# Kernel tuning notes

Measured on AMD Instinct MI355X. Metric: run time of the kernel, lower is better.

Reference implementation:

```python
import jax, jax.numpy as jnp
import numpy as np

N = 100000
E = 1600000
D = 128      # input_dim == hidden_dim
C = 40       # output_dim
L = 3        # num_layers
EPS = 1e-12  # F.normalize eps


def setup_inputs() -> dict:
    key = jax.random.key(0)
    ks = jax.random.split(key, 8)
    x = jax.random.normal(ks[0], (N, D), dtype=jnp.float32)
    edge_index = jax.random.randint(ks[1], (2, E), 0, N, dtype=jnp.int64)
    s = 1.0 / np.sqrt(D)
    # SAGEConv: lin_l (neighbor path, with bias), lin_r (root path, no bias)
    Wl = jax.random.uniform(ks[2], (L, D, D), jnp.float32, -s, s)
    bl = jax.random.uniform(ks[3], (L, D), jnp.float32, -s, s)
    Wr = jax.random.uniform(ks[4], (L, D, D), jnp.float32, -s, s)
    Wlin = jax.random.uniform(ks[5], (C, D), jnp.float32, -s, s)
    blin = jax.random.uniform(ks[6], (C,), jnp.float32, -s, s)
    return {"x": x, "edge_index": edge_index, "Wl": Wl, "bl": bl,
            "Wr": Wr, "Wlin": Wlin, "blin": blin}


def reference(x, edge_index, Wl, bl, Wr, Wlin, blin):
    src, dst = edge_index[0], edge_index[1]
    # in-degree counts for mean aggregation (computed once, reused per layer)
    cnt = jax.ops.segment_sum(jnp.ones((E,), jnp.float32), dst, num_segments=N)
    inv_cnt = (1.0 / jnp.maximum(cnt, 1.0))[:, None]  # [N,1]
    z = x
    for i in range(L):
        msg = z[src]  # gather [E, D]
        agg = jax.ops.segment_sum(msg, dst, num_segments=N) * inv_cnt  # mean [N, D]
        out = agg @ Wl[i].T + bl[i] + z @ Wr[i].T
        # SAGEConv normalize=True: L2 normalize per node
        nrm = jnp.linalg.norm(out, axis=-1, keepdims=True)
        out = out / jnp.maximum(nrm, EPS)
        z = jax.nn.relu(out)  # dropout p=0 -> identity
    return z @ Wlin.T + blin  # [N, C]
```

## Files before the change

### kernel.cpp

```cpp
#include <hip/hip_runtime.h>


typedef __bf16 bf16x8 __attribute__((ext_vector_type(8)));
typedef float  f32x4  __attribute__((ext_vector_type(4)));

#define MFMA16(a, b, c) __builtin_amdgcn_mfma_f32_16x16x32_bf16((a), (b), (c), 0, 0, 0)

__device__ __forceinline__ unsigned rne_bf16(float f) {
  unsigned u = __float_as_uint(f);
  unsigned r = u + 0x7FFFu + ((u >> 16) & 1u);
  return r >> 16;
}

__device__ __forceinline__ float bf_lo(unsigned u) { return __uint_as_float(u << 16); }
__device__ __forceinline__ float bf_hi(unsigned u) { return __uint_as_float(u & 0xFFFF0000u); }

__global__ __launch_bounds__(256) void prep_k(
    const float* __restrict__ x, const float* __restrict__ Wl,
    const float* __restrict__ Wr, const float* __restrict__ Wlin,
    uint2* __restrict__ planeA, unsigned short* __restrict__ wfrag,
    unsigned short* __restrict__ wlf, int* __restrict__ gcur,
    int cap, int n4) {
  const int b = blockIdx.x;
  const int tid = threadIdx.x;
  if (b == 0) {
    if (tid < 128) gcur[tid] = tid * cap;
    return;
  }
  if (b <= 96) {
    int id = (b - 1) * 256 + tid;
    int l = id & 63;
    int c = (id >> 6) & 7;
    int t = (id >> 9) & 7;
    int p = (id >> 12) & 1;
    int layer = id >> 13;
    int col = t * 16 + (l & 15);
    int kbase = c * 32 + (l >> 4) * 8;
    unsigned short* dst = wfrag + (size_t)layer * 65536 +
                          ((((size_t)p * 8 + t) * 8 + c) * 64 + l) * 8;
#pragma unroll
    for (int j = 0; j < 8; ++j) {
      int k = kbase + j;
      float w = (k < 128) ? Wl[layer * 16384 + col * 128 + k]
                          : Wr[layer * 16384 + col * 128 + (k - 128)];
      unsigned h = rne_bf16(w);
      unsigned o;
      if (p == 0) o = h;
      else o = rne_bf16(w - __uint_as_float(h << 16));
      dst[j] = (unsigned short)o;
    }
    return;
  }
  if (b == 97) {
    for (int id = tid; id < 3 * 4 * 64; id += 256) {
      int l = id & 63;
      int c = (id >> 6) & 3;
      int t = id >> 8;
      int col = t * 16 + (l & 15);
      int kbase = c * 32 + (l >> 4) * 8;
      unsigned short* dst = wlf + (size_t)id * 8;
#pragma unroll
      for (int j = 0; j < 8; ++j) {
        float w = (col < 40) ? Wlin[col * 128 + kbase + j] : 0.f;
        dst[j] = (unsigned short)rne_bf16(w);
      }
    }
    return;
  }
  int i = (b - 98) * 256 + tid;
  if (i >= n4) return;
  float4 f = ((const float4*)x)[i];
  uint2 o;
  o.x = rne_bf16(f.x) | (rne_bf16(f.y) << 16);
  o.y = rne_bf16(f.z) | (rne_bf16(f.w) << 16);
  planeA[i] = o;
}


__global__ __launch_bounds__(256) void bucketA_k(
    const int* __restrict__ src, const int* __restrict__ dst,
    int* __restrict__ gcur, unsigned* __restrict__ coarse, int E, int nc) {
  __shared__ int hist[128];
  __shared__ int sd[128];
  __shared__ int lpos[128];
  __shared__ int gbase[128];
  __shared__ unsigned stage[2048];
  __shared__ unsigned char sbuck[2048];

  const int tid = threadIdx.x;
  const int e0 = blockIdx.x * 2048;

  if (tid < 128) hist[tid] = 0;
  __syncthreads();

  int bv[8], pk[8];
#pragma unroll
  for (int j = 0; j < 8; ++j) {
    int e = e0 + j * 256 + tid;
    bv[j] = -1;
    if (e < E) {
      int s = src[e], d = dst[e];
      bv[j] = d >> 10;
      pk[j] = s | ((d & 1023) << 17);
      atomicAdd(&hist[bv[j]], 1);
    }
  }
  __syncthreads();

  if (tid < 128) sd[tid] = hist[tid];
  __syncthreads();
  for (int off = 1; off < 128; off <<= 1) {
    int t = 0;
    if (tid < 128 && tid >= off) t = sd[tid - off];
    __syncthreads();
    if (tid < 128) sd[tid] += t;
    __syncthreads();
  }
  if (tid < 128) {
    int excl = sd[tid] - hist[tid];
    lpos[tid] = excl;
    gbase[tid] = (tid < nc && hist[tid] > 0) ? atomicAdd(&gcur[tid], hist[tid]) : 0;
  }
  __syncthreads();

#pragma unroll
  for (int j = 0; j < 8; ++j) {
    if (bv[j] >= 0) {
      int slot = atomicAdd(&lpos[bv[j]], 1);
      stage[slot] = (unsigned)pk[j];
      sbuck[slot] = (unsigned char)bv[j];
    }
  }
  __syncthreads();

  const int total = sd[127];
  for (int i = tid; i < total; i += 256) {
    int b = sbuck[i];
    int excl = sd[b] - hist[b];
    coarse[gbase[b] + (i - excl)] = stage[i];
  }
}

__global__ __launch_bounds__(256) void bucketB_k(
    const int* __restrict__ gcur, const unsigned* __restrict__ coarse, int cap,
    int* __restrict__ esrc, int* __restrict__ offsets,
    float* __restrict__ inv_cnt, int n, int nc) {
  __shared__ int hcnt[1024];
  __shared__ int cur[1024];
  __shared__ int sd[256];
  __shared__ int sh_gdst;

  const int tid = threadIdx.x;
  const int b = blockIdx.x;
  const int base = b * 1024;
  const int nn = (n - base < 1024) ? (n - base) : 1024;
  const int wbeg = b * cap;
  const int wend = gcur[b];

  if (tid < 128) {
    int v = (tid < nc) ? (gcur[tid] - tid * cap) : 0;
    sd[tid] = v;
  }
  __syncthreads();
  for (int off = 1; off < 128; off <<= 1) {
    int u = 0;
    if (tid < 128 && tid >= off) u = sd[tid - off];
    __syncthreads();
    if (tid < 128) sd[tid] += u;
    __syncthreads();
  }
  if (tid == b) sh_gdst = sd[tid] - (wend - wbeg);
  for (int j = tid; j < 1024; j += 256) hcnt[j] = 0;
  __syncthreads();
  const int gdst = sh_gdst;

  for (int idx = wbeg + tid; idx < wend; idx += 256)
    atomicAdd(&hcnt[coarse[idx] >> 17], 1);
  __syncthreads();

  int b0 = hcnt[tid * 4], b1 = hcnt[tid * 4 + 1];
  int b2 = hcnt[tid * 4 + 2], b3 = hcnt[tid * 4 + 3];
  int tot = b0 + b1 + b2 + b3;
  sd[tid] = tot;
  __syncthreads();
  for (int off = 1; off < 256; off <<= 1) {
    int u = (tid >= off) ? sd[tid - off] : 0;
    __syncthreads();
    sd[tid] += u;
    __syncthreads();
  }
  int excl = gdst + sd[tid] - tot;
  cur[tid * 4]     = excl;
  cur[tid * 4 + 1] = excl + b0;
  cur[tid * 4 + 2] = excl + b0 + b1;
  cur[tid * 4 + 3] = excl + b0 + b1 + b2;
  __syncthreads();

  for (int j = tid; j < nn; j += 256) {
    offsets[base + j] = cur[j];
    int c = hcnt[j] > 1 ? hcnt[j] : 1;
    inv_cnt[base + j] = 1.0f / (float)c;
  }
  if (tid == 0 && base + nn >= n) offsets[n] = gdst + (wend - wbeg);
  __syncthreads();

  for (int idx = wbeg + tid; idx < wend; idx += 256) {
    unsigned p = coarse[idx];
    int pos = atomicAdd(&cur[p >> 17], 1);
    esrc[pos] = (int)(p & 0x1FFFFu);
  }
}

__global__ void aggregate_k(const unsigned short* __restrict__ zb,
                            const int* __restrict__ offsets,
                            const int* __restrict__ esrc,
                            const float* __restrict__ inv_cnt,
                            unsigned short* __restrict__ aggh, int n) {
  int node = (blockIdx.x * 256 + threadIdx.x) >> 4;
  int l16 = threadIdx.x & 15;
  if (node >= n) return;
  int beg = offsets[node], end = offsets[node + 1];
  float a0 = 0.f, a1 = 0.f, a2 = 0.f, a3 = 0.f;
  float a4 = 0.f, a5 = 0.f, a6 = 0.f, a7 = 0.f;
  int t = beg;
  for (; t + 4 <= end; t += 4) {
    int s0 = esrc[t], s1 = esrc[t + 1], s2 = esrc[t + 2], s3 = esrc[t + 3];
    uint4 d0 = *(const uint4*)(zb + (size_t)s0 * 128 + l16 * 8);
    uint4 d1 = *(const uint4*)(zb + (size_t)s1 * 128 + l16 * 8);
    uint4 d2 = *(const uint4*)(zb + (size_t)s2 * 128 + l16 * 8);
    uint4 d3 = *(const uint4*)(zb + (size_t)s3 * 128 + l16 * 8);
    a0 += bf_lo(d0.x); a1 += bf_hi(d0.x); a2 += bf_lo(d0.y); a3 += bf_hi(d0.y);
    a4 += bf_lo(d0.z); a5 += bf_hi(d0.z); a6 += bf_lo(d0.w); a7 += bf_hi(d0.w);
    a0 += bf_lo(d1.x); a1 += bf_hi(d1.x); a2 += bf_lo(d1.y); a3 += bf_hi(d1.y);
    a4 += bf_lo(d1.z); a5 += bf_hi(d1.z); a6 += bf_lo(d1.w); a7 += bf_hi(d1.w);
    a0 += bf_lo(d2.x); a1 += bf_hi(d2.x); a2 += bf_lo(d2.y); a3 += bf_hi(d2.y);
    a4 += bf_lo(d2.z); a5 += bf_hi(d2.z); a6 += bf_lo(d2.w); a7 += bf_hi(d2.w);
    a0 += bf_lo(d3.x); a1 += bf_hi(d3.x); a2 += bf_lo(d3.y); a3 += bf_hi(d3.y);
    a4 += bf_lo(d3.z); a5 += bf_hi(d3.z); a6 += bf_lo(d3.w); a7 += bf_hi(d3.w);
  }
  for (; t + 2 <= end; t += 2) {
    int s0 = esrc[t], s1 = esrc[t + 1];
    uint4 d0 = *(const uint4*)(zb + (size_t)s0 * 128 + l16 * 8);
    uint4 d1 = *(const uint4*)(zb + (size_t)s1 * 128 + l16 * 8);
    a0 += bf_lo(d0.x); a1 += bf_hi(d0.x); a2 += bf_lo(d0.y); a3 += bf_hi(d0.y);
    a4 += bf_lo(d0.z); a5 += bf_hi(d0.z); a6 += bf_lo(d0.w); a7 += bf_hi(d0.w);
    a0 += bf_lo(d1.x); a1 += bf_hi(d1.x); a2 += bf_lo(d1.y); a3 += bf_hi(d1.y);
    a4 += bf_lo(d1.z); a5 += bf_hi(d1.z); a6 += bf_lo(d1.w); a7 += bf_hi(d1.w);
  }
  if (t < end) {
    int s0 = esrc[t];
    uint4 d0 = *(const uint4*)(zb + (size_t)s0 * 128 + l16 * 8);
    a0 += bf_lo(d0.x); a1 += bf_hi(d0.x); a2 += bf_lo(d0.y); a3 += bf_hi(d0.y);
    a4 += bf_lo(d0.z); a5 += bf_hi(d0.z); a6 += bf_lo(d0.w); a7 += bf_hi(d0.w);
  }
  float ic = inv_cnt[node];
  uint4 hv;
  hv.x = rne_bf16(a0 * ic) | (rne_bf16(a1 * ic) << 16);
  hv.y = rne_bf16(a2 * ic) | (rne_bf16(a3 * ic) << 16);
  hv.z = rne_bf16(a4 * ic) | (rne_bf16(a5 * ic) << 16);
  hv.w = rne_bf16(a6 * ic) | (rne_bf16(a7 * ic) << 16);
  *(uint4*)(aggh + (size_t)node * 128 + l16 * 8) = hv;
}

template <bool FUSE>
__global__ __launch_bounds__(256) void sage_layer_mfma_k(
    const unsigned short* __restrict__ zb, const unsigned short* __restrict__ aggh,
    const unsigned short* __restrict__ wf, const float* __restrict__ bl,
    unsigned short* __restrict__ out_bf,
    const unsigned short* __restrict__ wlf, const float* __restrict__ blin,
    float* __restrict__ fout, int n, int ntiles) {
  __shared__ unsigned short Ah_s[32 * 256];
  __shared__ unsigned short Zt_s[32 * 128];
  __shared__ float psum[2][4][16];

  const int lane = threadIdx.x & 63;
  const int wv = threadIdx.x >> 6;
  const int g = lane >> 4;
  const int rl = lane & 15;

  const bf16x8* wfv = (const bf16x8*)wf;
  const int t0 = wv * 2, t1 = wv * 2 + 1;
  bf16x8 Bh0[8], Bh1[8], Bl0[8], Bl1[8];
#pragma unroll
  for (int c = 0; c < 8; ++c) {
    Bh0[c] = wfv[((0 * 8 + t0) * 8 + c) * 64 + lane];
    Bh1[c] = wfv[((0 * 8 + t1) * 8 + c) * 64 + lane];
    Bl0[c] = wfv[((1 * 8 + t0) * 8 + c) * 64 + lane];
    Bl1[c] = wfv[((1 * 8 + t1) * 8 + c) * 64 + lane];
  }
  const float b0 = bl[t0 * 16 + rl];
  const float b1 = bl[t1 * 16 + rl];

  char* pAh = (char*)Ah_s;
  char* pZt = (char*)Zt_s;
  const bf16x8* wlfv = (const bf16x8*)wlf;

  for (int tile = blockIdx.x; tile < ntiles; tile += gridDim.x) {
    const int v0 = tile * 32;

#pragma unroll
    for (int q = 0; q < 2; ++q) {
      int lin = q * 2048 + threadIdx.x * 8;
      int r = lin >> 7;
      int col = lin & 127;
      int v = v0 + r; v = (v < n) ? v : (n - 1);
      int swz = (r & 7) << 4;
      uint4 dh = *(const uint4*)(aggh + (size_t)v * 128 + col);
      uint4 dz = *(const uint4*)(zb + (size_t)v * 128 + col);
      *(uint4*)(pAh + ((r * 512 + col * 2) ^ swz)) = dh;
      *(uint4*)(pAh + ((r * 512 + 256 + col * 2) ^ swz)) = dz;
    }
    __syncthreads();

#pragma unroll
    for (int s = 0; s < 2; ++s) {
      f32x4 a0 = {0.f, 0.f, 0.f, 0.f};
      f32x4 a1 = {0.f, 0.f, 0.f, 0.f};
      const int rowH = (s * 16 + rl) * 512;
      const int swz = (rl & 7) << 4;
#pragma unroll
      for (int c = 0; c < 8; ++c) {
        int offH = (rowH + c * 64 + g * 16) ^ swz;
        bf16x8 ah = *(const bf16x8*)(pAh + offH);
        a0 = MFMA16(ah, Bh0[c], a0); a1 = MFMA16(ah, Bh1[c], a1);
        a0 = MFMA16(ah, Bl0[c], a0); a1 = MFMA16(ah, Bl1[c], a1);
      }
      float pr[4];
#pragma unroll
      for (int j = 0; j < 4; ++j) {
        a0[j] += b0; a1[j] += b1;
        pr[j] = a0[j] * a0[j] + a1[j] * a1[j];
      }
#pragma unroll
      for (int m = 1; m < 16; m <<= 1) {
#pragma unroll
        for (int j = 0; j < 4; ++j) pr[j] += __shfl_xor(pr[j], m);
      }
      if (rl == 0) {
#pragma unroll
        for (int j = 0; j < 4; ++j) psum[s][wv][g * 4 + j] = pr[j];
      }
      __syncthreads();
#pragma unroll
      for (int j = 0; j < 4; ++j) {
        int row16 = g * 4 + j;
        float tot = psum[s][0][row16] + psum[s][1][row16] +
                    psum[s][2][row16] + psum[s][3][row16];
        float inv = 1.0f / fmaxf(sqrtf(tot), 1e-12f);
        int v = v0 + s * 16 + row16;
        float o0 = fmaxf(a0[j] * inv, 0.f);
        float o1 = fmaxf(a1[j] * inv, 0.f);
        unsigned short q0 = (unsigned short)rne_bf16(o0);
        unsigned short q1 = (unsigned short)rne_bf16(o1);
        if (!FUSE) {
          if (v < n) {
            out_bf[(size_t)v * 128 + t0 * 16 + rl] = q0;
            out_bf[(size_t)v * 128 + t1 * 16 + rl] = q1;
          }
        } else {
          int rloc = s * 16 + row16;
          int sw = (rloc & 7) << 4;
          *(unsigned short*)(pZt + ((rloc * 256 + (t0 * 16 + rl) * 2) ^ sw)) = q0;
          *(unsigned short*)(pZt + ((rloc * 256 + (t1 * 16 + rl) * 2) ^ sw)) = q1;
        }
      }
    }

    if (FUSE) {
      __syncthreads();
      for (int job = wv; job < 6; job += 4) {
        int s = job / 3, t = job % 3;
        f32x4 acc = {0.f, 0.f, 0.f, 0.f};
        const int rowz = s * 16 + rl;
        const int swzz = (rowz & 7) << 4;
#pragma unroll
        for (int c = 0; c < 4; ++c) {
          bf16x8 a = *(const bf16x8*)(pZt + ((rowz * 256 + c * 64 + g * 16) ^ swzz));
          bf16x8 bw = wlfv[(t * 4 + c) * 64 + lane];
          acc = MFMA16(a, bw, acc);
        }
        int col = t * 16 + rl;
        if (col < 40) {
          float bb = blin[col];
#pragma unroll
          for (int j = 0; j < 4; ++j) {
            int v = v0 + s * 16 + g * 4 + j;
            if (v < n) fout[(size_t)v * 40 + col] = acc[j] + bb;
          }
        }
      }
    }
    __syncthreads();
  }
}


extern "C" void kernel_launch(void* const* d_in, const int* in_sizes, int n_in,
                              void* d_out, int out_size, void* d_ws, size_t ws_size,
                              hipStream_t stream) {
  const float* x    = (const float*)d_in[0];
  const int*   ei   = (const int*)d_in[1];
  const float* Wl   = (const float*)d_in[2];
  const float* bl   = (const float*)d_in[3];
  const float* Wr   = (const float*)d_in[4];
  const float* Wlin = (const float*)d_in[5];
  const float* blin = (const float*)d_in[6];

  const int N = in_sizes[0] / 128;
  const int E = in_sizes[1] / 2;
  const int D = 128;
  const int NC = (N + 1023) >> 10;
  const int cap = (E + NC - 1) / NC + 4096;

  const int* src = ei;
  const int* dstp = ei + E;

  unsigned short* planeA = (unsigned short*)d_ws;
  unsigned short* planeB = planeA + (size_t)N * D;
  unsigned short* aggh   = planeB + (size_t)N * D;
  float* inv_cnt = (float*)(aggh + (size_t)N * D);
  unsigned short* wlf = (unsigned short*)(inv_cnt + N);
  unsigned short* Wfrag = wlf + 6144;
  int*   offsets = (int*)(Wfrag + 3 * 65536);
  int*   esrc    = offsets + N + 1;
  unsigned* coarse = (unsigned*)(esrc + E);
  int*   gcur    = (int*)(coarse + (size_t)NC * cap);

  const int n4 = N * 32;
  prep_k<<<98 + (n4 + 255) / 256, 256, 0, stream>>>(
      x, Wl, Wr, Wlin, (uint2*)planeA, Wfrag, wlf, gcur, cap, n4);

  bucketA_k<<<(E + 2047) / 2048, 256, 0, stream>>>(src, dstp, gcur, coarse, E, NC);
  bucketB_k<<<NC, 256, 0, stream>>>(gcur, coarse, cap, esrc, offsets, inv_cnt, N, NC);

  const int aggGrid = (N * 16 + 255) / 256;
  const int ntiles = (N + 31) / 32;

  aggregate_k<<<aggGrid, 256, 0, stream>>>(planeA, offsets, esrc, inv_cnt, aggh, N);
  sage_layer_mfma_k<false><<<ntiles, 256, 0, stream>>>(
      planeA, aggh, Wfrag + 0 * 65536, bl + 0 * D, planeB, wlf, blin, nullptr, N, ntiles);
  aggregate_k<<<aggGrid, 256, 0, stream>>>(planeB, offsets, esrc, inv_cnt, aggh, N);
  sage_layer_mfma_k<false><<<ntiles, 256, 0, stream>>>(
      planeB, aggh, Wfrag + 1 * 65536, bl + 1 * D, planeA, wlf, blin, nullptr, N, ntiles);
  aggregate_k<<<aggGrid, 256, 0, stream>>>(planeA, offsets, esrc, inv_cnt, aggh, N);
  sage_layer_mfma_k<true><<<ntiles, 256, 0, stream>>>(
      planeA, aggh, Wfrag + 2 * 65536, bl + 2 * D, nullptr, wlf, blin,
      (float*)d_out, N, ntiles);
}
```

Before: 366.8 us.

## Load SAGE tiles via direct global-to-LDS loads and use persistent grid

Replaces the register-staged copy of aggregated and root features into shared memory with global_load_lds 16-byte direct loads. The swizzle is moved to the source address side. The dense-layer kernel now launches a fixed grid of 1024 blocks that loop over tiles, which amortizes the weight-fragment register loads across tiles. It also shrinks the unused Zt shared buffer for non-fused layers to lift occupancy. The risks are less latency hiding, since loads are not overlapped with compute across tiles, and correctness of the LDS layout mapping.

```diff
diff --git a/kernel.cpp b/kernel.cpp
--- a/kernel.cpp
+++ b/kernel.cpp
@@ -14,6 +14,12 @@
 
 __device__ __forceinline__ float bf_lo(unsigned u) { return __uint_as_float(u << 16); }
 __device__ __forceinline__ float bf_hi(unsigned u) { return __uint_as_float(u & 0xFFFF0000u); }
+
+__device__ __forceinline__ void gload_lds16(const void* g, void* l) {
+  __builtin_amdgcn_global_load_lds(
+      (const __attribute__((address_space(1))) unsigned int*)g,
+      (__attribute__((address_space(3))) unsigned int*)l, 16, 0, 0);
+}
 
 __global__ __launch_bounds__(256) void prep_k(
     const float* __restrict__ x, const float* __restrict__ Wl,
@@ -270,7 +276,7 @@
     const unsigned short* __restrict__ wlf, const float* __restrict__ blin,
     float* __restrict__ fout, int n, int ntiles) {
   __shared__ unsigned short Ah_s[32 * 256];
-  __shared__ unsigned short Zt_s[32 * 128];
+  __shared__ unsigned short Zt_s[FUSE ? 32 * 128 : 8];
   __shared__ float psum[2][4][16];
 
   const int lane = threadIdx.x & 63;
@@ -295,20 +301,22 @@
   char* pZt = (char*)Zt_s;
   const bf16x8* wlfv = (const bf16x8*)wlf;
 
+  const int rsub = lane >> 5;
+  const int hlf = (lane >> 4) & 1;
+  const int b16 = lane & 15;
+
   for (int tile = blockIdx.x; tile < ntiles; tile += gridDim.x) {
     const int v0 = tile * 32;
 
 #pragma unroll
-    for (int q = 0; q < 2; ++q) {
-      int lin = q * 2048 + threadIdx.x * 8;
-      int r = lin >> 7;
-      int col = lin & 127;
+    for (int q = 0; q < 4; ++q) {
+      int wq = wv * 4 + q;
+      int r = wq * 2 + rsub;
       int v = v0 + r; v = (v < n) ? v : (n - 1);
-      int swz = (r & 7) << 4;
-      uint4 dh = *(const uint4*)(aggh + (size_t)v * 128 + col);
-      uint4 dz = *(const uint4*)(zb + (size_t)v * 128 + col);
-      *(uint4*)(pAh + ((r * 512 + col * 2) ^ swz)) = dh;
-      *(uint4*)(pAh + ((r * 512 + 256 + col * 2) ^ swz)) = dz;
+      int sblk = b16 ^ (r & 7);
+      const unsigned short* srcp =
+          (hlf ? zb : aggh) + (size_t)v * 128 + sblk * 8;
+      gload_lds16(srcp, pAh + wq * 1024);
     }
     __syncthreads();
 
@@ -435,15 +443,16 @@
 
   const int aggGrid = (N * 16 + 255) / 256;
   const int ntiles = (N + 31) / 32;
+  const int sageGrid = 1024;
 
   aggregate_k<<<aggGrid, 256, 0, stream>>>(planeA, offsets, esrc, inv_cnt, aggh, N);
-  sage_layer_mfma_k<false><<<ntiles, 256, 0, stream>>>(
+  sage_layer_mfma_k<false><<<sageGrid, 256, 0, stream>>>(
       planeA, aggh, Wfrag + 0 * 65536, bl + 0 * D, planeB, wlf, blin, nullptr, N, ntiles);
   aggregate_k<<<aggGrid, 256, 0, stream>>>(planeB, offsets, esrc, inv_cnt, aggh, N);
-  sage_layer_mfma_k<false><<<ntiles, 256, 0, stream>>>(
+  sage_layer_mfma_k<false><<<sageGrid, 256, 0, stream>>>(
       planeB, aggh, Wfrag + 1 * 65536, bl + 1 * D, planeA, wlf, blin, nullptr, N, ntiles);
   aggregate_k<<<aggGrid, 256, 0, stream>>>(planeA, offsets, esrc, inv_cnt, aggh, N);
-  sage_layer_mfma_k<true><<<ntiles, 256, 0, stream>>>(
+  sage_layer_mfma_k<true><<<sageGrid, 256, 0, stream>>>(
       planeA, aggh, Wfrag + 2 * 65536, bl + 2 * D, nullptr, wlf, blin,
       (float*)d_out, N, ntiles);
 }
```

After: 352.5 us. -3.9%, faster.
